# Optimization experiments

Hardware: AMD Instinct MI355X
Metric: run time of the kernel (lower is better)

The kernel has to match this reference:

```python
import jax, jax.numpy as jnp
import numpy as np
from itertools import combinations

N = 40        # number of vectors
D = 5         # ambient dim
WIDTH = 128   # channel width
N_HIDDEN = 2  # hidden GeneralLinear layers


def _partition_labels(k):
    # restricted-growth strings = set partitions of range(k)
    out = []
    def rec(prefix):
        if len(prefix) == k:
            out.append(tuple(prefix)); return
        m = (max(prefix) + 1) if prefix else 0
        for v in range(m + 1):
            rec(prefix + [v])
    rec([])
    return out


def _canon(lab):
    m = {}
    return tuple(m.setdefault(v, len(m)) for v in lab)


def _indicator(lab, n):
    # T[i0..ik-1] = 1 iff equality pattern of indices matches the partition exactly
    k = len(lab)
    ax = [np.arange(n).reshape([n if i == a else 1 for i in range(k)]) for a in range(k)]
    T = np.ones((n,) * k, dtype=bool)
    for a, b in combinations(range(k), 2):
        eq = ax[a] == ax[b]
        T &= eq if lab[a] == lab[b] else ~eq
    return T.astype(np.float32)


def perm_invariant_basis(k, n, swappable=()):
    labs = _partition_labels(k)
    if not swappable:
        return jnp.asarray(np.stack([_indicator(l, n) for l in labs]))
    (a, b), = swappable
    tensors, seen = [], set()
    for lab in labs:
        sl = list(lab); sl[a], sl[b] = sl[b], sl[a]
        sl = _canon(sl)
        if lab in seen or sl in seen:
            continue
        seen.add(lab); seen.add(sl)
        T = _indicator(lab, n)
        if sl != lab:
            T = T + _indicator(sl, n)  # symmetrize over the swappable index pair
        tensors.append(T)
    return jnp.asarray(np.stack(tensors))


def _gl4(basis, W, bw, bias_basis, x):
    # GeneralLinear on 2-tensor channels.
    # basis: (K,n,n,n,n)  x: (in,n,n)  W: (out,in,K)  bw: (out,Kb)  bias_basis: (Kb,n,n)
    t = jnp.einsum('kabcd,icd->ikab', basis, x)          # (in,K,n,n)
    out = jnp.einsum('oik,ikab->oab', W, t)
    return out + jnp.einsum('om,mab->oab', bw, bias_basis)


def setup_inputs() -> dict:
    key = jax.random.key(0)
    ks = jax.random.split(key, 10)
    basis_sym_nonsym = perm_invariant_basis(4, N, ((0, 1),))  # (11,n,n,n,n)
    basis_nonsym = perm_invariant_basis(4, N)                  # (15,n,n,n,n)
    bias_basis = perm_invariant_basis(2, N)                    # (2,n,n)
    K_sym = basis_sym_nonsym.shape[0]
    K_full = basis_nonsym.shape[0]
    K_b = bias_basis.shape[0]
    s = 0.02
    f32 = jnp.float32
    return {
        'S': jax.random.normal(ks[0], (N, D), f32),
        'basis_sym_nonsym': basis_sym_nonsym,
        'basis_nonsym': basis_nonsym,
        'bias_basis': bias_basis,
        'W0': jax.random.normal(ks[1], (WIDTH, 1, K_sym), f32) * s,
        'b0': jax.random.normal(ks[2], (WIDTH, K_b), f32) * s,
        'Wh': jax.random.normal(ks[3], (N_HIDDEN, WIDTH, WIDTH, K_full), f32) * s,
        'bh': jax.random.normal(ks[4], (N_HIDDEN, WIDTH, K_b), f32) * s,
        'Wp': jax.random.normal(ks[5], (1, WIDTH, K_sym), f32) * s,
        'bp': jax.random.normal(ks[6], (1, K_b), f32) * s,
        'Wi': jax.random.normal(ks[7], (1, WIDTH, K_b), f32) * s,
        'bi': jax.random.normal(ks[8], (1, 1), f32) * s,
    }


def reference(S, basis_sym_nonsym, basis_nonsym, bias_basis, W0, b0, Wh, bh, Wp, bp, Wi, bi):
    n, d = S.shape
    X = (S @ S.T)[None]                                               # (1,n,n) Gram matrix
    X = jax.nn.leaky_relu(_gl4(basis_sym_nonsym, W0, b0, bias_basis, X))
    for l in range(Wh.shape[0]):
        X = jax.nn.leaky_relu(_gl4(basis_nonsym, Wh[l], bh[l], bias_basis, X))
    basis_nonsym_sym = jnp.transpose(basis_sym_nonsym, (0, 3, 4, 1, 2))
    pairs = _gl4(basis_nonsym_sym, Wp, bp, bias_basis, X)[0]          # (n,n)
    # identity head: order-2 basis fully contracts X to a scalar; bias_basis=ones((1,1))
    identity_scalar = jnp.einsum('oik,kab,iab->o', Wi, bias_basis, X) + bi[:, 0]  # (1,)
    # A[c,d] = sum_ab pairs[a,b] S[a,c] S[b,d]  (== einsum('ab,abcd->cd', pairs, S(x)S))
    A = jnp.einsum('ab,ac,bd->cd', pairs, S, S) + identity_scalar * jnp.eye(d, dtype=S.dtype)
    _, eigvecs = jnp.linalg.eigh(A)
    u = eigvecs[:, -1]                                                # top eigenvector
    return S @ u
```

## Files before the change

kernel.cpp:

```cpp
#include <hip/hip_runtime.h>
#include <math.h>

#define NPTS 40
#define NN   1600
#define WID  128
#define NPAIR 780

#define ST_D  0
#define ST_R  5120
#define ST_C  10240
#define ST_TR 15360
#define ST_T  15488
#define ST_SIZE 16384

#define VT_VA   0
#define VT_VB   5120
#define VT_VDG  10240
#define VT_SOFF 15360
#define VT_SDG  15488
#define VT_SIZE 15616

#define PVA 0
#define PVB 40
#define PDG 80
#define PSOFF 120
#define PSDG 121

#define CM_SZ1 16384
#define CM_SIZE (15*16384)

#define WS_XTA   0
#define WS_XTB   204800
#define WS_STA   409600
#define WS_STB   425984
#define WS_STC   442368
#define WS_CM0   458752
#define WS_CM1   704512
#define WS_VT1   950272
#define WS_VT2   965888
#define WS_VTP   981504
#define WS_PRAW  981632
#define WS_TOTAL 983232

static __device__ __forceinline__ float lrelu(float v) {
    return v >= 0.f ? v : 0.01f * v;
}

static __device__ __forceinline__ void pair_decode(int q, int& a, int& b) {
    int aa = 0, rem = q;
    while (rem >= 39 - aa) { rem -= 39 - aa; ++aa; }
    a = aa; b = aa + 1 + rem;
}

__global__ __launch_bounds__(256) void k_l0c(
    const float* __restrict__ S, const float* __restrict__ W0, const float* __restrict__ b0,
    const float* __restrict__ Wh,
    float* __restrict__ XT, float* __restrict__ st,
    float* __restrict__ cm0, float* __restrict__ cm1)
{
    const int tid = threadIdx.x;
    const int o = blockIdx.x;

    {
        const int idx = blockIdx.x * 256 + tid;
        const int l = idx >> 14;
        const int r2 = idx & 16383;
        const int oo = r2 >> 7;
        const int ii = r2 & 127;
        const float* w = Wh + ((l * WID + oo) * WID + ii) * 15;
        float* cm = l ? cm1 : cm0;
        const int base = ii * 128 + oo;
        const float w0=w[0],w1=w[1],w2=w[2],w3=w[3],w4=w[4],w5=w[5],w6=w[6],w7=w[7],
                    w8=w[8],w9=w[9],w10=w[10],w11=w[11],w12=w[12],w13=w[13],w14=w[14];
        cm[ 0*CM_SZ1+base] = w6 - w7 - w12 + w14;
        cm[ 1*CM_SZ1+base] = w8 - w10 - w11 + w14;
        cm[ 2*CM_SZ1+base] = w5 - w7 - w11 - w13 + 2.f*w14;
        cm[ 3*CM_SZ1+base] = w9 - w10 - w12 - w13 + 2.f*w14;
        cm[ 4*CM_SZ1+base] = w7 - w14;
        cm[ 5*CM_SZ1+base] = w10 - w14;
        cm[ 6*CM_SZ1+base] = w11 - w14;
        cm[ 7*CM_SZ1+base] = w12 - w14;
        cm[ 8*CM_SZ1+base] = w0 - w1 - w2 - w3 + 2.f*w4;
        cm[ 9*CM_SZ1+base] = w1 - w4;
        cm[10*CM_SZ1+base] = w2 - w4;
        cm[11*CM_SZ1+base] = w13 - w14;
        cm[12*CM_SZ1+base] = w14;
        cm[13*CM_SZ1+base] = w3 - w4;
        cm[14*CM_SZ1+base] = w4;
    }

    __shared__ float sS[NPTS * 5];
    __shared__ float sX[NN];
    __shared__ float sP[NN];
    __shared__ float sR[NPTS], sC[NPTS], sD[NPTS], sTT[2];

    for (int t = tid; t < NPTS * 5; t += 256) sS[t] = S[t];
    __syncthreads();
    for (int p = tid; p < NN; p += 256) {
        int a = p / NPTS, b = p % NPTS;
        float acc = 0.f;
#pragma unroll
        for (int k = 0; k < 5; ++k) acc += sS[a * 5 + k] * sS[b * 5 + k];
        sX[p] = acc;
    }
    __syncthreads();
    if (tid < NPTS) {
        float r = 0.f, c = 0.f;
        for (int j = 0; j < NPTS; ++j) { r += sX[tid * NPTS + j]; c += sX[j * NPTS + tid]; }
        sR[tid] = r; sC[tid] = c; sD[tid] = sX[tid * 41];
    }
    __syncthreads();
    if (tid == 0) {
        float tr = 0.f, T = 0.f;
        for (int a = 0; a < NPTS; ++a) { tr += sD[a]; T += sR[a]; }
        sTT[0] = tr; sTT[1] = T;
    }
    __syncthreads();

    float w[11];
#pragma unroll
    for (int k = 0; k < 11; ++k) w[k] = W0[o * 11 + k];
    const float tr = sTT[0], T = sTT[1];
    const float cfX = w[6] - w[7] - w[8] + w[10];
    const float cfd = w[5] - w[7] - w[8] - w[9] + 2.f * w[10];
    const float cfR = w[7] - w[10];
    const float cfC = w[8] - w[10];
    const float so  = w[9] * tr + w[10] * (T - tr) + b0[o * 2 + 1];
    const float cdd = w[0] - w[1] - w[2] - w[3] + 2.f * w[4];
    const float cdR = w[1] - w[4];
    const float cdC = w[2] - w[4];
    const float sd  = w[3] * tr + w[4] * (T - tr) + b0[o * 2 + 0];

    for (int p = tid; p < NN; p += 256) {
        int a = p / NPTS, b = p % NPTS;
        float v;
        if (a == b) {
            v = cdd * sD[a] + cdR * sR[a] + cdC * sC[a] + sd;
        } else {
            float xs = sX[p] + sX[b * NPTS + a];
            v = cfX * xs + cfd * (sD[a] + sD[b]) + cfR * (sR[a] + sR[b]) + cfC * (sC[a] + sC[b]) + so;
        }
        sP[p] = lrelu(v);
    }
    __syncthreads();
    for (int p = tid; p < NN; p += 256) XT[p * WID + o] = sP[p];
    if (tid < NPTS) {
        float r = 0.f, c = 0.f;
        for (int j = 0; j < NPTS; ++j) { r += sP[tid * NPTS + j]; c += sP[j * NPTS + tid]; }
        st[ST_D + o * NPTS + tid] = sP[tid * 41];
        st[ST_R + o * NPTS + tid] = r;
        st[ST_C + o * NPTS + tid] = c;
        sR[tid] = r; sD[tid] = sP[tid * 41];
    }
    __syncthreads();
    if (tid == 0) {
        float t2 = 0.f, T2 = 0.f;
        for (int a = 0; a < NPTS; ++a) { t2 += sD[a]; T2 += sR[a]; }
        st[ST_TR + o] = t2; st[ST_T + o] = T2;
    }
}

template<bool COMP>
__global__ __launch_bounds__(256) void k_sv(
    const float* __restrict__ XT, const float* __restrict__ stIn,
    float* __restrict__ stOut,
    const float* __restrict__ cm, const float* __restrict__ bias,
    float* __restrict__ vt)
{
    const int tid = threadIdx.x;
    const int i = tid & 127, h = tid >> 7;
    const int a = blockIdx.x;
    __shared__ float sD[128], sR[128], sC[128], sTr[128], sT[128];
    __shared__ float part[2][2][128];
    __shared__ float vpart[3][2][128];

    if (a < 40) {
        if (COMP) {
            float r = 0.f, c = 0.f;
            for (int b = h * 20; b < h * 20 + 20; ++b) {
                r += XT[(a * 40 + b) * WID + i];
                c += XT[(b * 40 + a) * WID + i];
            }
            part[0][h][i] = r; part[1][h][i] = c;
            __syncthreads();
            if (tid < 128) {
                sR[i] = part[0][0][i] + part[0][1][i];
                sC[i] = part[1][0][i] + part[1][1][i];
                sD[i] = XT[(a * 41) * WID + i];
                stOut[ST_D + i * 40 + a] = sD[i];
                stOut[ST_R + i * 40 + a] = sR[i];
                stOut[ST_C + i * 40 + a] = sC[i];
            }
        } else {
            if (tid < 128) {
                sD[i] = stIn[ST_D + i * 40 + a];
                sR[i] = stIn[ST_R + i * 40 + a];
                sC[i] = stIn[ST_C + i * 40 + a];
            }
            __syncthreads();
        }
        __syncthreads();
        const int o = i;
        float acca = 0.f, accb = 0.f, accg = 0.f;
        for (int k = h * 64; k < h * 64 + 64; ++k) {
            const float d = sD[k], r = sR[k], c = sC[k];
            acca += cm[ 2*CM_SZ1 + k*128 + o] * d + cm[ 4*CM_SZ1 + k*128 + o] * r + cm[ 6*CM_SZ1 + k*128 + o] * c;
            accb += cm[ 3*CM_SZ1 + k*128 + o] * d + cm[ 5*CM_SZ1 + k*128 + o] * r + cm[ 7*CM_SZ1 + k*128 + o] * c;
            accg += cm[ 8*CM_SZ1 + k*128 + o] * d + cm[ 9*CM_SZ1 + k*128 + o] * r + cm[10*CM_SZ1 + k*128 + o] * c;
        }
        vpart[0][h][o] = acca; vpart[1][h][o] = accb; vpart[2][h][o] = accg;
        __syncthreads();
        if (tid < 128) {
            vt[VT_VA  + a * 128 + o] = vpart[0][0][o] + vpart[0][1][o];
            vt[VT_VB  + a * 128 + o] = vpart[1][0][o] + vpart[1][1][o];
            vt[VT_VDG + a * 128 + o] = vpart[2][0][o] + vpart[2][1][o];
        }
    } else {
        if (COMP) {
            float tt = 0.f;
            for (int p = h * 800; p < (h + 1) * 800; ++p) tt += XT[p * WID + i];
            part[0][h][i] = tt;
            __syncthreads();
            if (tid < 128) {
                sT[i] = part[0][0][i] + part[0][1][i];
                float trv = 0.f;
                for (int a2 = 0; a2 < 40; ++a2) trv += XT[(a2 * 41) * WID + i];
                sTr[i] = trv;
                stOut[ST_TR + i] = trv; stOut[ST_T + i] = sT[i];
            }
        } else {
            if (tid < 128) { sTr[i] = stIn[ST_TR + i]; sT[i] = stIn[ST_T + i]; }
            __syncthreads();
        }
        __syncthreads();
        const int o = i;
        float soff = 0.f, sdg = 0.f;
        for (int k = h * 64; k < h * 64 + 64; ++k) {
            const float trv = sTr[k], Tv = sT[k];
            soff += cm[11*CM_SZ1 + k*128 + o] * trv + cm[12*CM_SZ1 + k*128 + o] * Tv;
            sdg  += cm[13*CM_SZ1 + k*128 + o] * trv + cm[14*CM_SZ1 + k*128 + o] * Tv;
        }
        vpart[0][h][o] = soff; vpart[1][h][o] = sdg;
        __syncthreads();
        if (tid < 128) {
            vt[VT_SOFF + o] = vpart[0][0][o] + vpart[0][1][o] + bias[o * 2 + 1];
            vt[VT_SDG  + o] = vpart[1][0][o] + vpart[1][1][o] + bias[o * 2 + 0];
        }
    }
}

__global__ __launch_bounds__(256) void k_hid(
    const float* __restrict__ XTin, float* __restrict__ XTout,
    const float* __restrict__ cm, const float* __restrict__ vt)
{
    const int tid = threadIdx.x;
    const int blk = blockIdx.x;
    if (blk == 390) {
        const int o = tid & 127, h = tid >> 7;
        const float sdg = vt[VT_SDG + o];
        for (int a = h; a < 40; a += 2)
            XTout[(a * 41) * WID + o] = lrelu(vt[VT_VDG + a * 128 + o] + sdg);
        return;
    }
    __shared__ float sxab[2][128], sxba[2][128];
    const int j = tid >> 7, o = tid & 127;
    int aa, bb;
    pair_decode(blk * 2 + j, aa, bb);
    const int p = aa * 40 + bb, pt = bb * 40 + aa;
    sxab[j][o] = XTin[p * WID + o];
    sxba[j][o] = XTin[pt * WID + o];
    __syncthreads();

    float acc1 = 0.f, acc2 = 0.f;
#pragma unroll 8
    for (int i2 = 0; i2 < 128; ++i2) {
        const float c1v = cm[i2 * 128 + o];
        const float c2v = cm[CM_SZ1 + i2 * 128 + o];
        const float xab = sxab[j][i2];
        const float xba = sxba[j][i2];
        acc1 += c1v * xab + c2v * xba;
        acc2 += c1v * xba + c2v * xab;
    }
    const float soff = vt[VT_SOFF + o];
    XTout[p * WID + o]  = lrelu(acc1 + vt[VT_VA + aa * 128 + o] + vt[VT_VB + bb * 128 + o] + soff);
    XTout[pt * WID + o] = lrelu(acc2 + vt[VT_VA + bb * 128 + o] + vt[VT_VB + aa * 128 + o] + soff);
}

__global__ __launch_bounds__(256) void k_svp(
    const float* __restrict__ XT, float* __restrict__ stOut,
    const float* __restrict__ Wp, const float* __restrict__ bp,
    float* __restrict__ vtp, float* __restrict__ praw)
{
    const int tid = threadIdx.x;
    const int i = tid & 127, h = tid >> 7;
    const int blk = blockIdx.x;
    __shared__ float sD[128], sR[128], sC[128];
    __shared__ float part[2][2][128];
    __shared__ float red[3][128];

    if (blk < 40) {
        const int a = blk;
        float r = 0.f, c = 0.f;
        for (int b = h * 20; b < h * 20 + 20; ++b) {
            r += XT[(a * 40 + b) * WID + i];
            c += XT[(b * 40 + a) * WID + i];
        }
        part[0][h][i] = r; part[1][h][i] = c;
        __syncthreads();
        if (tid < 128) {
            sR[i] = part[0][0][i] + part[0][1][i];
            sC[i] = part[1][0][i] + part[1][1][i];
            sD[i] = XT[(a * 41) * WID + i];
            stOut[ST_D + i * 40 + a] = sD[i];
            stOut[ST_R + i * 40 + a] = sR[i];
            stOut[ST_C + i * 40 + a] = sC[i];
        }
        __syncthreads();
        if (tid < 128) {
            const float* pw = Wp + i * 11;
            const float p0=pw[0],p1=pw[1],p2=pw[2],p3=pw[3],p4=pw[4],p5=pw[5],
                        p7=pw[7],p8=pw[8],p9=pw[9],p10=pw[10];
            const float cpa = p1 - p4 - 2.f*p7 + 2.f*p10;
            const float cpb = p2 - p4 - 2.f*p8 + 2.f*p10;
            const float cra = p7 - p10;
            const float crb = p8 - p10;
            const float cddp = p0 - p3 - 2.f*p5 + 2.f*p9;
            const float crcp = p5 - p9;
            const float rc = sR[i] + sC[i];
            red[0][i] = cpa * sD[i] + cra * rc;
            red[1][i] = cpb * sD[i] + crb * rc;
            red[2][i] = cddp * sD[i] + crcp * rc;
        }
        __syncthreads();
        for (int s = 64; s > 0; s >>= 1) {
            if (tid < s) {
                red[0][tid] += red[0][tid + s];
                red[1][tid] += red[1][tid + s];
                red[2][tid] += red[2][tid + s];
            }
            __syncthreads();
        }
        if (tid == 0) {
            vtp[PVA + a] = red[0][0];
            vtp[PVB + a] = red[1][0];
            vtp[PDG + a] = red[2][0];
        }
    } else if (blk == 40) {
        float tt = 0.f;
        for (int p = h * 800; p < (h + 1) * 800; ++p) tt += XT[p * WID + i];
        part[0][h][i] = tt;
        __syncthreads();
        if (tid < 128) {
            const float Tv = part[0][0][i] + part[0][1][i];
            float trv = 0.f;
            for (int a2 = 0; a2 < 40; ++a2) trv += XT[(a2 * 41) * WID + i];
            stOut[ST_TR + i] = trv; stOut[ST_T + i] = Tv;
            const float p3 = Wp[i*11+3], p4 = Wp[i*11+4], p9 = Wp[i*11+9], p10 = Wp[i*11+10];
            red[0][i] = (p4 - p10) * trv + p10 * Tv;
            red[1][i] = (p3 - p9) * trv + p9 * Tv;
        }
        __syncthreads();
        for (int s = 64; s > 0; s >>= 1) {
            if (tid < s) { red[0][tid] += red[0][tid + s]; red[1][tid] += red[1][tid + s]; }
            __syncthreads();
        }
        if (tid == 0) {
            vtp[PSOFF] = red[0][0] + bp[1];
            vtp[PSDG]  = red[1][0] + bp[0];
        }
    } else {
        int aa, bb;
        pair_decode(blk - 41, aa, bb);
        const int p = aa * 40 + bb, pt = bb * 40 + aa;
        if (tid < 128) {
            const float p6 = Wp[i*11+6], p7 = Wp[i*11+7], p8 = Wp[i*11+8], p10 = Wp[i*11+10];
            red[0][i] = (p6 - p7 - p8 + p10) * (XT[p * WID + i] + XT[pt * WID + i]);
        }
        __syncthreads();
        for (int s = 64; s > 0; s >>= 1) {
            if (tid < s) red[0][tid] += red[0][tid + s];
            __syncthreads();
        }
        if (tid == 0) { praw[p] = red[0][0]; praw[pt] = red[0][0]; }
    }
}

__global__ __launch_bounds__(256) void k_final(
    const float* __restrict__ S, const float* __restrict__ praw,
    const float* __restrict__ vtp,
    const float* __restrict__ st, const float* __restrict__ Wi,
    const float* __restrict__ bi, float* __restrict__ out)
{
    __shared__ float sS[NPTS * 5];
    __shared__ float sPr[NN];
    __shared__ float M1[5][NPTS];
    __shared__ float sA[25];
    __shared__ float sIsc;
    __shared__ double sU[5];
    const int tid = threadIdx.x;

    for (int t = tid; t < NPTS * 5; t += 256) sS[t] = S[t];
    for (int p = tid; p < NN; p += 256) {
        const int a = p / NPTS, b = p % NPTS;
        float v;
        if (a == b) v = vtp[PDG + a] + vtp[PSDG];
        else        v = praw[p] + vtp[PVA + a] + vtp[PVB + b] + vtp[PSOFF];
        sPr[p] = v;
    }
    __syncthreads();

    if (tid < 200) {
        const int c = tid / NPTS, b = tid % NPTS;
        float acc = 0.f;
        for (int a = 0; a < NPTS; ++a) acc += sS[a * 5 + c] * sPr[a * NPTS + b];
        M1[c][b] = acc;
    }
    if (tid == 255) {
        float s = 0.f;
        for (int i = 0; i < WID; ++i) {
            const float tri = st[ST_TR + i], Ti = st[ST_T + i];
            s += Wi[i * 2 + 0] * tri + Wi[i * 2 + 1] * (Ti - tri);
        }
        sIsc = s + bi[0];
    }
    __syncthreads();
    if (tid < 25) {
        const int c = tid / 5, d = tid % 5;
        float acc = 0.f;
        for (int b = 0; b < NPTS; ++b) acc += M1[c][b] * sS[b * 5 + d];
        sA[tid] = acc;
    }
    __syncthreads();

    if (tid == 0) {
        double A[5][5], V[5][5];
        for (int c = 0; c < 5; ++c)
            for (int d = 0; d < 5; ++d)
                A[c][d] = (double)((c >= d) ? sA[c * 5 + d] : sA[d * 5 + c]);
        for (int c = 0; c < 5; ++c) A[c][c] += (double)sIsc;
        for (int c = 0; c < 5; ++c)
            for (int d = 0; d < 5; ++d) V[c][d] = (c == d) ? 1.0 : 0.0;

        double dscale = 1.0;
        for (int c = 0; c < 5; ++c) dscale += A[c][c] * A[c][c];
        for (int sweep = 0; sweep < 30; ++sweep) {
            double off = 0.0;
            for (int p = 0; p < 4; ++p)
                for (int q = p + 1; q < 5; ++q) off += A[p][q] * A[p][q];
            if (off < 1e-26 * dscale) break;
            for (int p = 0; p < 4; ++p) {
                for (int q = p + 1; q < 5; ++q) {
                    const double apq = A[p][q];
                    if (fabs(apq) < 1e-300) continue;
                    const double theta = (A[q][q] - A[p][p]) / (2.0 * apq);
                    const double t = (theta >= 0.0 ? 1.0 : -1.0) / (fabs(theta) + sqrt(theta * theta + 1.0));
                    const double c = 1.0 / sqrt(t * t + 1.0);
                    const double s = t * c;
                    for (int k = 0; k < 5; ++k) {
                        const double akp = A[k][p], akq = A[k][q];
                        A[k][p] = c * akp - s * akq;
                        A[k][q] = s * akp + c * akq;
                    }
                    for (int k = 0; k < 5; ++k) {
                        const double apk = A[p][k], aqk = A[q][k];
                        A[p][k] = c * apk - s * aqk;
                        A[q][k] = s * apk + c * aqk;
                    }
                    for (int k = 0; k < 5; ++k) {
                        const double vkp = V[k][p], vkq = V[k][q];
                        V[k][p] = c * vkp - s * vkq;
                        V[k][q] = s * vkp + c * vkq;
                    }
                }
            }
        }
        int best = 0;
        for (int k = 1; k < 5; ++k) if (A[k][k] > A[best][best]) best = k;
        double u[5];
        for (int k = 0; k < 5; ++k) u[k] = V[k][best];
        int jm = 0; double am = fabs(u[0]);
        for (int k = 1; k < 5; ++k) if (fabs(u[k]) > am) { am = fabs(u[k]); jm = k; }
        if (u[jm] < 0.0) for (int k = 0; k < 5; ++k) u[k] = -u[k];
        for (int k = 0; k < 5; ++k) sU[k] = u[k];
    }
    __syncthreads();
    if (tid < NPTS) {
        float acc = 0.f;
#pragma unroll
        for (int k = 0; k < 5; ++k) acc += sS[tid * 5 + k] * (float)sU[k];
        out[tid] = acc;
    }
}

extern "C" void kernel_launch(void* const* d_in, const int* in_sizes, int n_in,
                              void* d_out, int out_size, void* d_ws, size_t ws_size,
                              hipStream_t stream) {
    const float* S  = (const float*)d_in[0];
    const float* W0 = (const float*)d_in[4];
    const float* b0 = (const float*)d_in[5];
    const float* Wh = (const float*)d_in[6];
    const float* bh = (const float*)d_in[7];
    const float* Wp = (const float*)d_in[8];
    const float* bp = (const float*)d_in[9];
    const float* Wi = (const float*)d_in[10];
    const float* bi = (const float*)d_in[11];
    float* out = (float*)d_out;
    float* ws = (float*)d_ws;
    if (ws_size < (size_t)WS_TOTAL * sizeof(float)) return;

    float* XTA = ws + WS_XTA;
    float* XTB = ws + WS_XTB;
    float* stA = ws + WS_STA;
    float* stB = ws + WS_STB;
    float* stC = ws + WS_STC;
    float* cm0 = ws + WS_CM0;
    float* cm1 = ws + WS_CM1;
    float* vt1 = ws + WS_VT1;
    float* vt2 = ws + WS_VT2;
    float* vtp = ws + WS_VTP;
    float* praw = ws + WS_PRAW;

    k_l0c<<<WID, 256, 0, stream>>>(S, W0, b0, Wh, XTA, stA, cm0, cm1);
    k_sv<false><<<41, 256, 0, stream>>>(XTA, stA, stB, cm0, bh, vt1);
    k_hid<<<391, 256, 0, stream>>>(XTA, XTB, cm0, vt1);
    k_sv<true><<<41, 256, 0, stream>>>(XTB, stB, stB, cm1, bh + 2 * WID, vt2);
    k_hid<<<391, 256, 0, stream>>>(XTB, XTA, cm1, vt2);
    k_svp<<<821, 256, 0, stream>>>(XTA, stC, Wp, bp, vtp, praw);
    k_final<<<1, 256, 0, stream>>>(S, praw, vtp, stC, Wi, bi, out);
}
```

Before: 134.0 us.

## Fuse hidden layers, stats, projection head and eigen solve into three kernels

Merges the per-layer statistics/vector kernels into the hidden-layer kernels, so each of the 390 blocks recomputes the needed row/column/diagonal reductions and cm-weighted vectors for its own endpoints. The projection head and final eigen solve are folded into the second hidden kernel, which uses atomics and a last-block counter instead of separate launches. This cuts the launch count from seven to three and removes the intermediate dependency bubbles. In exchange, the cm-weighted vector work is done redundantly in every block, and the change adds atomic reductions plus a single-block tail.

After: 179.3 us. 1.34x slower.

```diff
diff --git a/kernel.cpp b/kernel.cpp
--- a/kernel.cpp
+++ b/kernel.cpp
@@ -4,43 +4,32 @@
 #define NPTS 40
 #define NN   1600
 #define WID  128
-#define NPAIR 780
 
 #define ST_D  0
 #define ST_R  5120
 #define ST_C  10240
 #define ST_TR 15360
 #define ST_T  15488
-#define ST_SIZE 16384
-
-#define VT_VA   0
-#define VT_VB   5120
-#define VT_VDG  10240
-#define VT_SOFF 15360
-#define VT_SDG  15488
-#define VT_SIZE 15616
+
+#define CM_SZ1 16384
 
 #define PVA 0
 #define PVB 40
 #define PDG 80
-#define PSOFF 120
-#define PSDG 121
-
-#define CM_SZ1 16384
-#define CM_SIZE (15*16384)
+#define A_SOFF 120
+#define A_SDG  121
+#define A_ISC  122
 
 #define WS_XTA   0
 #define WS_XTB   204800
 #define WS_STA   409600
-#define WS_STB   425984
-#define WS_STC   442368
-#define WS_CM0   458752
-#define WS_CM1   704512
-#define WS_VT1   950272
-#define WS_VT2   965888
-#define WS_VTP   981504
-#define WS_PRAW  981632
-#define WS_TOTAL 983232
+#define WS_CM0   425984
+#define WS_CM1   671744
+#define WS_T1    917504
+#define WS_ACC   917632
+#define WS_PRAW  917760
+#define WS_CNT   919360
+#define WS_TOTAL 919424
 
 static __device__ __forceinline__ float lrelu(float v) {
     return v >= 0.f ? v : 0.01f * v;
@@ -56,13 +45,20 @@
     const float* __restrict__ S, const float* __restrict__ W0, const float* __restrict__ b0,
     const float* __restrict__ Wh,
     float* __restrict__ XT, float* __restrict__ st,
-    float* __restrict__ cm0, float* __restrict__ cm1)
+    float* __restrict__ cm0, float* __restrict__ cm1,
+    float* __restrict__ T1, float* __restrict__ accb, unsigned int* __restrict__ cnt)
 {
     const int tid = threadIdx.x;
     const int o = blockIdx.x;
 
+    if (o == 0) {
+        if (tid < 128) T1[tid] = 0.f;
+        if (tid >= 128) accb[tid - 128] = 0.f;
+        if (tid == 0) *cnt = 0u;
+    }
+
     {
-        const int idx = blockIdx.x * 256 + tid;
+        const int idx = o * 256 + tid;
         const int l = idx >> 14;
         const int r2 = idx & 16383;
         const int oo = r2 >> 7;
@@ -106,7 +102,7 @@
     __syncthreads();
     if (tid < NPTS) {
         float r = 0.f, c = 0.f;
-        for (int j = 0; j < NPTS; ++j) { r += sX[tid * NPTS + j]; c += sX[j * NPTS + tid]; }
+        for (int jj = 0; jj < NPTS; ++jj) { r += sX[tid * NPTS + jj]; c += sX[jj * NPTS + tid]; }
         sR[tid] = r; sC[tid] = c; sD[tid] = sX[tid * 41];
     }
     __syncthreads();
@@ -146,7 +142,7 @@
     for (int p = tid; p < NN; p += 256) XT[p * WID + o] = sP[p];
     if (tid < NPTS) {
         float r = 0.f, c = 0.f;
-        for (int j = 0; j < NPTS; ++j) { r += sP[tid * NPTS + j]; c += sP[j * NPTS + tid]; }
+        for (int jj = 0; jj < NPTS; ++jj) { r += sP[tid * NPTS + jj]; c += sP[jj * NPTS + tid]; }
         st[ST_D + o * NPTS + tid] = sP[tid * 41];
         st[ST_R + o * NPTS + tid] = r;
         st[ST_C + o * NPTS + tid] = c;
@@ -160,284 +156,326 @@
     }
 }
 
-template<bool COMP>
-__global__ __launch_bounds__(256) void k_sv(
-    const float* __restrict__ XT, const float* __restrict__ stIn,
-    float* __restrict__ stOut,
-    const float* __restrict__ cm, const float* __restrict__ bias,
-    float* __restrict__ vt)
+__global__ __launch_bounds__(256) void k_hid1(
+    const float* __restrict__ XTA, const float* __restrict__ stA,
+    const float* __restrict__ cm, const float* __restrict__ bl,
+    float* __restrict__ XTB, float* __restrict__ T1)
 {
-    const int tid = threadIdx.x;
-    const int i = tid & 127, h = tid >> 7;
-    const int a = blockIdx.x;
-    __shared__ float sD[128], sR[128], sC[128], sTr[128], sT[128];
-    __shared__ float part[2][2][128];
-    __shared__ float vpart[3][2][128];
-
-    if (a < 40) {
-        if (COMP) {
+    const int tid = threadIdx.x, blk = blockIdx.x;
+    const int j = tid >> 7, o = tid & 127;
+    const bool diag = (blk < 40);
+    int e0, e1, e2, e3;
+    pair_decode(2 * blk, e0, e1);
+    pair_decode(2 * blk + 1, e2, e3);
+    const int epl[5] = { e0, e1, e2, e3, diag ? blk : 0 };
+    const int nep = diag ? 5 : 4;
+
+    __shared__ float sD[5][128], sR[5][128], sC[5][128], sTr[128], sT[128];
+    __shared__ float sxab[2][128], sxba[2][128];
+    __shared__ float vpart[11][2][128];
+    __shared__ float svt[11][128];
+
+    for (int t = tid; t < nep * 128; t += 256) {
+        const int e = t >> 7, k = t & 127, a = epl[e];
+        sD[e][k] = stA[ST_D + k * 40 + a];
+        sR[e][k] = stA[ST_R + k * 40 + a];
+        sC[e][k] = stA[ST_C + k * 40 + a];
+    }
+    if (tid < 128) { sTr[o] = stA[ST_TR + o]; sT[o] = stA[ST_T + o]; }
+    {
+        const int a = epl[2 * j], b = epl[2 * j + 1];
+        sxab[j][o] = XTA[(a * 40 + b) * 128 + o];
+        sxba[j][o] = XTA[(b * 40 + a) * 128 + o];
+    }
+    __syncthreads();
+
+    float fva0 = 0, fva1 = 0, fva2 = 0, fva3 = 0;
+    float fvb0 = 0, fvb1 = 0, fvb2 = 0, fvb3 = 0;
+    float fso = 0, fdg = 0, fsd = 0;
+    const int k0 = 64 * j;
+    for (int k = k0; k < k0 + 64; ++k) {
+        const int c = k * 128 + o;
+        const float m2 = cm[2*CM_SZ1+c], m3 = cm[3*CM_SZ1+c], m4 = cm[4*CM_SZ1+c],
+                    m5 = cm[5*CM_SZ1+c], m6 = cm[6*CM_SZ1+c], m7 = cm[7*CM_SZ1+c];
+        {
+            const float d = sD[0][k], r = sR[0][k], cc = sC[0][k];
+            fva0 += m2*d + m4*r + m6*cc; fvb0 += m3*d + m5*r + m7*cc;
+        }
+        {
+            const float d = sD[1][k], r = sR[1][k], cc = sC[1][k];
+            fva1 += m2*d + m4*r + m6*cc; fvb1 += m3*d + m5*r + m7*cc;
+        }
+        {
+            const float d = sD[2][k], r = sR[2][k], cc = sC[2][k];
+            fva2 += m2*d + m4*r + m6*cc; fvb2 += m3*d + m5*r + m7*cc;
+        }
+        {
+            const float d = sD[3][k], r = sR[3][k], cc = sC[3][k];
+            fva3 += m2*d + m4*r + m6*cc; fvb3 += m3*d + m5*r + m7*cc;
+        }
+        fso += cm[11*CM_SZ1+c] * sTr[k] + cm[12*CM_SZ1+c] * sT[k];
+        if (diag) {
+            fdg += cm[8*CM_SZ1+c]*sD[4][k] + cm[9*CM_SZ1+c]*sR[4][k] + cm[10*CM_SZ1+c]*sC[4][k];
+            fsd += cm[13*CM_SZ1+c]*sTr[k] + cm[14*CM_SZ1+c]*sT[k];
+        }
+    }
+    vpart[0][j][o]=fva0; vpart[1][j][o]=fva1; vpart[2][j][o]=fva2; vpart[3][j][o]=fva3;
+    vpart[4][j][o]=fvb0; vpart[5][j][o]=fvb1; vpart[6][j][o]=fvb2; vpart[7][j][o]=fvb3;
+    vpart[8][j][o]=fso; vpart[9][j][o]=fdg; vpart[10][j][o]=fsd;
+    __syncthreads();
+    if (tid < 128) {
+        for (int m = 0; m < 8; ++m) svt[m][o] = vpart[m][0][o] + vpart[m][1][o];
+        svt[8][o]  = vpart[8][0][o] + vpart[8][1][o] + bl[o * 2 + 1];
+        svt[9][o]  = vpart[9][0][o] + vpart[9][1][o];
+        svt[10][o] = vpart[10][0][o] + vpart[10][1][o] + bl[o * 2 + 0];
+    }
+    __syncthreads();
+
+    float acc1 = 0.f, acc2 = 0.f;
+#pragma unroll 8
+    for (int i = 0; i < 128; ++i) {
+        const float c1v = cm[i * 128 + o];
+        const float c2v = cm[CM_SZ1 + i * 128 + o];
+        const float xab = sxab[j][i], xba = sxba[j][i];
+        acc1 += c1v * xab + c2v * xba;
+        acc2 += c1v * xba + c2v * xab;
+    }
+    const int a = epl[2 * j], b = epl[2 * j + 1];
+    const float so = svt[8][o];
+    const float o1 = lrelu(acc1 + svt[2 * j][o]     + svt[4 + 2 * j + 1][o] + so);
+    const float o2 = lrelu(acc2 + svt[2 * j + 1][o] + svt[4 + 2 * j][o]     + so);
+    XTB[(a * 40 + b) * 128 + o] = o1;
+    XTB[(b * 40 + a) * 128 + o] = o2;
+    float xd = 0.f;
+    if (diag && j == 0) {
+        xd = lrelu(svt[9][o] + svt[10][o]);
+        XTB[(blk * 41) * 128 + o] = xd;
+    }
+    vpart[0][j][o] = o1 + o2 + xd;
+    __syncthreads();
+    if (tid < 128) atomicAdd(&T1[o], vpart[0][0][o] + vpart[0][1][o]);
+}
+
+__global__ __launch_bounds__(256) void k_hid2f(
+    const float* __restrict__ S,
+    const float* __restrict__ XTB, const float* __restrict__ T1,
+    const float* __restrict__ cm, const float* __restrict__ bl,
+    const float* __restrict__ Wp, const float* __restrict__ bp,
+    const float* __restrict__ Wi, const float* __restrict__ bi,
+    float* __restrict__ praw, float* __restrict__ accb, unsigned int* __restrict__ cnt,
+    float* __restrict__ out)
+{
+    const int tid = threadIdx.x, blk = blockIdx.x;
+    const int j = tid >> 7, o = tid & 127;
+    const bool diag = (blk < 40);
+    int e0, e1, e2, e3;
+    pair_decode(2 * blk, e0, e1);
+    pair_decode(2 * blk + 1, e2, e3);
+    const int epl[5] = { e0, e1, e2, e3, diag ? blk : 0 };
+    const int nep = diag ? 5 : 4;
+
+    __shared__ float sD[5][128], sR[5][128], sC[5][128], sTr[128], sT[128];
+    __shared__ float sxab[2][128], sxba[2][128];
+    __shared__ float vpart[11][2][128];
+    __shared__ float svt[11][128];
+    __shared__ float sxd[128];
+    __shared__ float rr[7][2][128];
+    __shared__ double dbuf[55];
+    __shared__ int sLast;
+
+    {
+        const int k = o, h = j;
+        for (int e = 0; e < nep; ++e) {
+            const int a = epl[e];
             float r = 0.f, c = 0.f;
-            for (int b = h * 20; b < h * 20 + 20; ++b) {
-                r += XT[(a * 40 + b) * WID + i];
-                c += XT[(b * 40 + a) * WID + i];
+            for (int b = 20 * h; b < 20 * h + 20; ++b) {
+                r += XTB[(a * 40 + b) * 128 + k];
+                c += XTB[(b * 40 + a) * 128 + k];
             }
-            part[0][h][i] = r; part[1][h][i] = c;
+            vpart[0][h][k] = r; vpart[1][h][k] = c;
             __syncthreads();
             if (tid < 128) {
-                sR[i] = part[0][0][i] + part[0][1][i];
-                sC[i] = part[1][0][i] + part[1][1][i];
-                sD[i] = XT[(a * 41) * WID + i];
-                stOut[ST_D + i * 40 + a] = sD[i];
-                stOut[ST_R + i * 40 + a] = sR[i];
-                stOut[ST_C + i * 40 + a] = sC[i];
-            }
-        } else {
-            if (tid < 128) {
-                sD[i] = stIn[ST_D + i * 40 + a];
-                sR[i] = stIn[ST_R + i * 40 + a];
-                sC[i] = stIn[ST_C + i * 40 + a];
+                sD[e][k] = XTB[(a * 41) * 128 + k];
+                sR[e][k] = vpart[0][0][k] + vpart[0][1][k];
+                sC[e][k] = vpart[1][0][k] + vpart[1][1][k];
             }
             __syncthreads();
         }
+        float t = 0.f;
+        for (int a2 = 20 * h; a2 < 20 * h + 20; ++a2) t += XTB[(a2 * 41) * 128 + k];
+        vpart[0][h][k] = t;
         __syncthreads();
-        const int o = i;
-        float acca = 0.f, accb = 0.f, accg = 0.f;
-        for (int k = h * 64; k < h * 64 + 64; ++k) {
-            const float d = sD[k], r = sR[k], c = sC[k];
-            acca += cm[ 2*CM_SZ1 + k*128 + o] * d + cm[ 4*CM_SZ1 + k*128 + o] * r + cm[ 6*CM_SZ1 + k*128 + o] * c;
-            accb += cm[ 3*CM_SZ1 + k*128 + o] * d + cm[ 5*CM_SZ1 + k*128 + o] * r + cm[ 7*CM_SZ1 + k*128 + o] * c;
-            accg += cm[ 8*CM_SZ1 + k*128 + o] * d + cm[ 9*CM_SZ1 + k*128 + o] * r + cm[10*CM_SZ1 + k*128 + o] * c;
-        }
-        vpart[0][h][o] = acca; vpart[1][h][o] = accb; vpart[2][h][o] = accg;
-        __syncthreads();
-        if (tid < 128) {
-            vt[VT_VA  + a * 128 + o] = vpart[0][0][o] + vpart[0][1][o];
-            vt[VT_VB  + a * 128 + o] = vpart[1][0][o] + vpart[1][1][o];
-            vt[VT_VDG + a * 128 + o] = vpart[2][0][o] + vpart[2][1][o];
-        }
-    } else {
-        if (COMP) {
-            float tt = 0.f;
-            for (int p = h * 800; p < (h + 1) * 800; ++p) tt += XT[p * WID + i];
-            part[0][h][i] = tt;
-            __syncthreads();
-            if (tid < 128) {
-                sT[i] = part[0][0][i] + part[0][1][i];
-                float trv = 0.f;
-                for (int a2 = 0; a2 < 40; ++a2) trv += XT[(a2 * 41) * WID + i];
-                sTr[i] = trv;
-                stOut[ST_TR + i] = trv; stOut[ST_T + i] = sT[i];
-            }
-        } else {
-            if (tid < 128) { sTr[i] = stIn[ST_TR + i]; sT[i] = stIn[ST_T + i]; }
-            __syncthreads();
-        }
-        __syncthreads();
-        const int o = i;
-        float soff = 0.f, sdg = 0.f;
-        for (int k = h * 64; k < h * 64 + 64; ++k) {
-            const float trv = sTr[k], Tv = sT[k];
-            soff += cm[11*CM_SZ1 + k*128 + o] * trv + cm[12*CM_SZ1 + k*128 + o] * Tv;
-            sdg  += cm[13*CM_SZ1 + k*128 + o] * trv + cm[14*CM_SZ1 + k*128 + o] * Tv;
-        }
-        vpart[0][h][o] = soff; vpart[1][h][o] = sdg;
-        __syncthreads();
-        if (tid < 128) {
-            vt[VT_SOFF + o] = vpart[0][0][o] + vpart[0][1][o] + bias[o * 2 + 1];
-            vt[VT_SDG  + o] = vpart[1][0][o] + vpart[1][1][o] + bias[o * 2 + 0];
-        }
-    }
-}
-
-__global__ __launch_bounds__(256) void k_hid(
-    const float* __restrict__ XTin, float* __restrict__ XTout,
-    const float* __restrict__ cm, const float* __restrict__ vt)
-{
-    const int tid = threadIdx.x;
-    const int blk = blockIdx.x;
-    if (blk == 390) {
-        const int o = tid & 127, h = tid >> 7;
-        const float sdg = vt[VT_SDG + o];
-        for (int a = h; a < 40; a += 2)
-            XTout[(a * 41) * WID + o] = lrelu(vt[VT_VDG + a * 128 + o] + sdg);
-        return;
-    }
-    __shared__ float sxab[2][128], sxba[2][128];
-    const int j = tid >> 7, o = tid & 127;
-    int aa, bb;
-    pair_decode(blk * 2 + j, aa, bb);
-    const int p = aa * 40 + bb, pt = bb * 40 + aa;
-    sxab[j][o] = XTin[p * WID + o];
-    sxba[j][o] = XTin[pt * WID + o];
+        if (tid < 128) { sTr[k] = vpart[0][0][k] + vpart[0][1][k]; sT[k] = T1[k]; }
+    }
+    {
+        const int a = epl[2 * j], b = epl[2 * j + 1];
+        sxab[j][o] = XTB[(a * 40 + b) * 128 + o];
+        sxba[j][o] = XTB[(b * 40 + a) * 128 + o];
+    }
+    __syncthreads();
+
+    float fva0 = 0, fva1 = 0, fva2 = 0, fva3 = 0;
+    float fvb0 = 0, fvb1 = 0, fvb2 = 0, fvb3 = 0;
+    float fso = 0, fdg = 0, fsd = 0;
+    const int k0 = 64 * j;
+    for (int k = k0; k < k0 + 64; ++k) {
+        const int c = k * 128 + o;
+        const float m2 = cm[2*CM_SZ1+c], m3 = cm[3*CM_SZ1+c], m4 = cm[4*CM_SZ1+c],
+                    m5 = cm[5*CM_SZ1+c], m6 = cm[6*CM_SZ1+c], m7 = cm[7*CM_SZ1+c];
+        {
+            const float d = sD[0][k], r = sR[0][k], cc = sC[0][k];
+            fva0 += m2*d + m4*r + m6*cc; fvb0 += m3*d + m5*r + m7*cc;
+        }
+        {
+            const float d = sD[1][k], r = sR[1][k], cc = sC[1][k];
+            fva1 += m2*d + m4*r + m6*cc; fvb1 += m3*d + m5*r + m7*cc;
+        }
+        {
+            const float d = sD[2][k], r = sR[2][k], cc = sC[2][k];
+            fva2 += m2*d + m4*r + m6*cc; fvb2 += m3*d + m5*r + m7*cc;
+        }
+        {
+            const float d = sD[3][k], r = sR[3][k], cc = sC[3][k];
+            fva3 += m2*d + m4*r + m6*cc; fvb3 += m3*d + m5*r + m7*cc;
+        }
+        fso += cm[11*CM_SZ1+c] * sTr[k] + cm[12*CM_SZ1+c] * sT[k];
+        if (diag) {
+            fdg += cm[8*CM_SZ1+c]*sD[4][k] + cm[9*CM_SZ1+c]*sR[4][k] + cm[10*CM_SZ1+c]*sC[4][k];
+            fsd += cm[13*CM_SZ1+c]*sTr[k] + cm[14*CM_SZ1+c]*sT[k];
+        }
+    }
+    vpart[0][j][o]=fva0; vpart[1][j][o]=fva1; vpart[2][j][o]=fva2; vpart[3][j][o]=fva3;
+    vpart[4][j][o]=fvb0; vpart[5][j][o]=fvb1; vpart[6][j][o]=fvb2; vpart[7][j][o]=fvb3;
+    vpart[8][j][o]=fso; vpart[9][j][o]=fdg; vpart[10][j][o]=fsd;
+    __syncthreads();
+    if (tid < 128) {
+        for (int m = 0; m < 8; ++m) svt[m][o] = vpart[m][0][o] + vpart[m][1][o];
+        svt[8][o]  = vpart[8][0][o] + vpart[8][1][o] + bl[o * 2 + 1];
+        svt[9][o]  = vpart[9][0][o] + vpart[9][1][o];
+        svt[10][o] = vpart[10][0][o] + vpart[10][1][o] + bl[o * 2 + 0];
+    }
     __syncthreads();
 
     float acc1 = 0.f, acc2 = 0.f;
 #pragma unroll 8
-    for (int i2 = 0; i2 < 128; ++i2) {
-        const float c1v = cm[i2 * 128 + o];
-        const float c2v = cm[CM_SZ1 + i2 * 128 + o];
-        const float xab = sxab[j][i2];
-        const float xba = sxba[j][i2];
+    for (int i = 0; i < 128; ++i) {
+        const float c1v = cm[i * 128 + o];
+        const float c2v = cm[CM_SZ1 + i * 128 + o];
+        const float xab = sxab[j][i], xba = sxba[j][i];
         acc1 += c1v * xab + c2v * xba;
         acc2 += c1v * xba + c2v * xab;
     }
-    const float soff = vt[VT_SOFF + o];
-    XTout[p * WID + o]  = lrelu(acc1 + vt[VT_VA + aa * 128 + o] + vt[VT_VB + bb * 128 + o] + soff);
-    XTout[pt * WID + o] = lrelu(acc2 + vt[VT_VA + bb * 128 + o] + vt[VT_VB + aa * 128 + o] + soff);
-}
-
-__global__ __launch_bounds__(256) void k_svp(
-    const float* __restrict__ XT, float* __restrict__ stOut,
-    const float* __restrict__ Wp, const float* __restrict__ bp,
-    float* __restrict__ vtp, float* __restrict__ praw)
-{
-    const int tid = threadIdx.x;
-    const int i = tid & 127, h = tid >> 7;
-    const int blk = blockIdx.x;
-    __shared__ float sD[128], sR[128], sC[128];
-    __shared__ float part[2][2][128];
-    __shared__ float red[3][128];
-
-    if (blk < 40) {
-        const int a = blk;
-        float r = 0.f, c = 0.f;
-        for (int b = h * 20; b < h * 20 + 20; ++b) {
-            r += XT[(a * 40 + b) * WID + i];
-            c += XT[(b * 40 + a) * WID + i];
-        }
-        part[0][h][i] = r; part[1][h][i] = c;
+    const int pa = epl[2 * j], pb = epl[2 * j + 1];
+    const float so = svt[8][o];
+    const float x1 = lrelu(acc1 + svt[2 * j][o]     + svt[4 + 2 * j + 1][o] + so);
+    const float x2 = lrelu(acc2 + svt[2 * j + 1][o] + svt[4 + 2 * j][o]     + so);
+    if (diag && j == 0) sxd[o] = lrelu(svt[9][o] + svt[10][o]);
+
+    const float p0 = Wp[o*11+0], p1 = Wp[o*11+1], p2 = Wp[o*11+2], p3 = Wp[o*11+3],
+                p4 = Wp[o*11+4], p5 = Wp[o*11+5], p6 = Wp[o*11+6], p7 = Wp[o*11+7],
+                p8 = Wp[o*11+8], p9 = Wp[o*11+9], p10 = Wp[o*11+10];
+    const float wi0 = Wi[o*2+0], wi1 = Wi[o*2+1];
+    const float s12 = x1 + x2;
+    rr[0][j][o] = (p6 - p7 - p8 + p10) * s12;
+    rr[1][j][o] = (p7 - p10) * s12;
+    rr[2][j][o] = (p8 - p10) * s12;
+    rr[3][j][o] = (p5 - p9) * s12;
+    rr[4][j][o] = p10 * s12;
+    rr[5][j][o] = p9 * s12;
+    rr[6][j][o] = wi1 * s12;
+    __syncthreads();
+    for (int stp = 64; stp > 0; stp >>= 1) {
+        if (o < stp) {
+            for (int m = 0; m < 7; ++m) rr[m][j][o] += rr[m][j][o + stp];
+        }
         __syncthreads();
-        if (tid < 128) {
-            sR[i] = part[0][0][i] + part[0][1][i];
-            sC[i] = part[1][0][i] + part[1][1][i];
-            sD[i] = XT[(a * 41) * WID + i];
-            stOut[ST_D + i * 40 + a] = sD[i];
-            stOut[ST_R + i * 40 + a] = sR[i];
-            stOut[ST_C + i * 40 + a] = sC[i];
-        }
+    }
+    if (o == 0) {
+        const float v = rr[0][j][0];
+        praw[pa * 40 + pb] = v;
+        praw[pb * 40 + pa] = v;
+        atomicAdd(&accb[PVA + pa], rr[1][j][0]); atomicAdd(&accb[PVA + pb], rr[1][j][0]);
+        atomicAdd(&accb[PVB + pa], rr[2][j][0]); atomicAdd(&accb[PVB + pb], rr[2][j][0]);
+        atomicAdd(&accb[PDG + pa], rr[3][j][0]); atomicAdd(&accb[PDG + pb], rr[3][j][0]);
+        atomicAdd(&accb[A_SOFF], rr[4][j][0]);
+        atomicAdd(&accb[A_SDG],  rr[5][j][0]);
+        atomicAdd(&accb[A_ISC],  rr[6][j][0]);
+    }
+    if (diag) {
         __syncthreads();
-        if (tid < 128) {
-            const float* pw = Wp + i * 11;
-            const float p0=pw[0],p1=pw[1],p2=pw[2],p3=pw[3],p4=pw[4],p5=pw[5],
-                        p7=pw[7],p8=pw[8],p9=pw[9],p10=pw[10];
-            const float cpa = p1 - p4 - 2.f*p7 + 2.f*p10;
-            const float cpb = p2 - p4 - 2.f*p8 + 2.f*p10;
-            const float cra = p7 - p10;
-            const float crb = p8 - p10;
-            const float cddp = p0 - p3 - 2.f*p5 + 2.f*p9;
-            const float crcp = p5 - p9;
-            const float rc = sR[i] + sC[i];
-            red[0][i] = cpa * sD[i] + cra * rc;
-            red[1][i] = cpb * sD[i] + crb * rc;
-            red[2][i] = cddp * sD[i] + crcp * rc;
-        }
+        const float xdv = (j == 0) ? sxd[o] : 0.f;
+        rr[0][j][o] = (p1 - p4) * xdv;
+        rr[1][j][o] = (p2 - p4) * xdv;
+        rr[2][j][o] = (p0 - p3) * xdv;
+        rr[3][j][o] = p4 * xdv;
+        rr[4][j][o] = p3 * xdv;
+        rr[5][j][o] = wi0 * xdv;
         __syncthreads();
-        for (int s = 64; s > 0; s >>= 1) {
-            if (tid < s) {
-                red[0][tid] += red[0][tid + s];
-                red[1][tid] += red[1][tid + s];
-                red[2][tid] += red[2][tid + s];
+        for (int stp = 64; stp > 0; stp >>= 1) {
+            if (o < stp) {
+                for (int m = 0; m < 6; ++m) rr[m][j][o] += rr[m][j][o + stp];
             }
             __syncthreads();
         }
         if (tid == 0) {
-            vtp[PVA + a] = red[0][0];
-            vtp[PVB + a] = red[1][0];
-            vtp[PDG + a] = red[2][0];
-        }
-    } else if (blk == 40) {
-        float tt = 0.f;
-        for (int p = h * 800; p < (h + 1) * 800; ++p) tt += XT[p * WID + i];
-        part[0][h][i] = tt;
-        __syncthreads();
-        if (tid < 128) {
-            const float Tv = part[0][0][i] + part[0][1][i];
-            float trv = 0.f;
-            for (int a2 = 0; a2 < 40; ++a2) trv += XT[(a2 * 41) * WID + i];
-            stOut[ST_TR + i] = trv; stOut[ST_T + i] = Tv;
-            const float p3 = Wp[i*11+3], p4 = Wp[i*11+4], p9 = Wp[i*11+9], p10 = Wp[i*11+10];
-            red[0][i] = (p4 - p10) * trv + p10 * Tv;
-            red[1][i] = (p3 - p9) * trv + p9 * Tv;
-        }
-        __syncthreads();
-        for (int s = 64; s > 0; s >>= 1) {
-            if (tid < s) { red[0][tid] += red[0][tid + s]; red[1][tid] += red[1][tid + s]; }
-            __syncthreads();
-        }
-        if (tid == 0) {
-            vtp[PSOFF] = red[0][0] + bp[1];
-            vtp[PSDG]  = red[1][0] + bp[0];
-        }
-    } else {
-        int aa, bb;
-        pair_decode(blk - 41, aa, bb);
-        const int p = aa * 40 + bb, pt = bb * 40 + aa;
-        if (tid < 128) {
-            const float p6 = Wp[i*11+6], p7 = Wp[i*11+7], p8 = Wp[i*11+8], p10 = Wp[i*11+10];
-            red[0][i] = (p6 - p7 - p8 + p10) * (XT[p * WID + i] + XT[pt * WID + i]);
-        }
-        __syncthreads();
-        for (int s = 64; s > 0; s >>= 1) {
-            if (tid < s) red[0][tid] += red[0][tid + s];
-            __syncthreads();
-        }
-        if (tid == 0) { praw[p] = red[0][0]; praw[pt] = red[0][0]; }
-    }
-}
-
-__global__ __launch_bounds__(256) void k_final(
-    const float* __restrict__ S, const float* __restrict__ praw,
-    const float* __restrict__ vtp,
-    const float* __restrict__ st, const float* __restrict__ Wi,
-    const float* __restrict__ bi, float* __restrict__ out)
-{
-    __shared__ float sS[NPTS * 5];
-    __shared__ float sPr[NN];
-    __shared__ float M1[5][NPTS];
-    __shared__ float sA[25];
-    __shared__ float sIsc;
-    __shared__ double sU[5];
-    const int tid = threadIdx.x;
-
-    for (int t = tid; t < NPTS * 5; t += 256) sS[t] = S[t];
+            atomicAdd(&accb[PVA + blk], rr[0][0][0]);
+            atomicAdd(&accb[PVB + blk], rr[1][0][0]);
+            atomicAdd(&accb[PDG + blk], rr[2][0][0]);
+            atomicAdd(&accb[A_SOFF], rr[3][0][0]);
+            atomicAdd(&accb[A_SDG],  rr[4][0][0]);
+            atomicAdd(&accb[A_ISC],  rr[5][0][0]);
+        }
+    }
+
+    __threadfence();
+    if (tid == 0) {
+        const unsigned old = atomicAdd(cnt, 1u);
+        sLast = (old == 389u) ? 1 : 0;
+    }
+    __syncthreads();
+    if (!sLast) return;
+    __threadfence();
+
+    float* sPr = &vpart[0][0][0];
+    float* M1  = &svt[0][0];
+    float* sSS = &sxab[0][0];
+    float* sA  = &sxd[0];
+
+    for (int t = tid; t < NPTS * 5; t += 256) sSS[t] = S[t];
+    const float psoff = accb[A_SOFF] + bp[1];
+    const float psdg  = accb[A_SDG]  + bp[0];
     for (int p = tid; p < NN; p += 256) {
         const int a = p / NPTS, b = p % NPTS;
         float v;
-        if (a == b) v = vtp[PDG + a] + vtp[PSDG];
-        else        v = praw[p] + vtp[PVA + a] + vtp[PVB + b] + vtp[PSOFF];
+        if (a == b) v = accb[PDG + a] + psdg;
+        else        v = praw[p] + accb[PVA + a] + accb[PVB + b] + psoff;
         sPr[p] = v;
     }
     __syncthreads();
-
     if (tid < 200) {
         const int c = tid / NPTS, b = tid % NPTS;
         float acc = 0.f;
-        for (int a = 0; a < NPTS; ++a) acc += sS[a * 5 + c] * sPr[a * NPTS + b];
-        M1[c][b] = acc;
-    }
-    if (tid == 255) {
-        float s = 0.f;
-        for (int i = 0; i < WID; ++i) {
-            const float tri = st[ST_TR + i], Ti = st[ST_T + i];
-            s += Wi[i * 2 + 0] * tri + Wi[i * 2 + 1] * (Ti - tri);
-        }
-        sIsc = s + bi[0];
+        for (int a = 0; a < NPTS; ++a) acc += sSS[a * 5 + c] * sPr[a * NPTS + b];
+        M1[c * NPTS + b] = acc;
     }
     __syncthreads();
     if (tid < 25) {
         const int c = tid / 5, d = tid % 5;
         float acc = 0.f;
-        for (int b = 0; b < NPTS; ++b) acc += M1[c][b] * sS[b * 5 + d];
+        for (int b = 0; b < NPTS; ++b) acc += M1[c * NPTS + b] * sSS[b * 5 + d];
         sA[tid] = acc;
     }
     __syncthreads();
 
     if (tid == 0) {
-        double A[5][5], V[5][5];
+        const float isc = accb[A_ISC] + bi[0];
+        double (*A)[5] = (double(*)[5])&dbuf[0];
+        double (*V)[5] = (double(*)[5])&dbuf[25];
+        double* sU = &dbuf[50];
         for (int c = 0; c < 5; ++c)
             for (int d = 0; d < 5; ++d)
                 A[c][d] = (double)((c >= d) ? sA[c * 5 + d] : sA[d * 5 + c]);
-        for (int c = 0; c < 5; ++c) A[c][c] += (double)sIsc;
+        for (int c = 0; c < 5; ++c) A[c][c] += (double)isc;
         for (int c = 0; c < 5; ++c)
             for (int d = 0; d < 5; ++d) V[c][d] = (c == d) ? 1.0 : 0.0;
 
@@ -454,22 +492,22 @@
                     if (fabs(apq) < 1e-300) continue;
                     const double theta = (A[q][q] - A[p][p]) / (2.0 * apq);
                     const double t = (theta >= 0.0 ? 1.0 : -1.0) / (fabs(theta) + sqrt(theta * theta + 1.0));
-                    const double c = 1.0 / sqrt(t * t + 1.0);
-                    const double s = t * c;
+                    const double cth = 1.0 / sqrt(t * t + 1.0);
+                    const double sth = t * cth;
                     for (int k = 0; k < 5; ++k) {
                         const double akp = A[k][p], akq = A[k][q];
-                        A[k][p] = c * akp - s * akq;
-                        A[k][q] = s * akp + c * akq;
+                        A[k][p] = cth * akp - sth * akq;
+                        A[k][q] = sth * akp + cth * akq;
                     }
                     for (int k = 0; k < 5; ++k) {
                         const double apk = A[p][k], aqk = A[q][k];
-                        A[p][k] = c * apk - s * aqk;
-                        A[q][k] = s * apk + c * aqk;
+                        A[p][k] = cth * apk - sth * aqk;
+                        A[q][k] = sth * apk + cth * aqk;
                     }
                     for (int k = 0; k < 5; ++k) {
                         const double vkp = V[k][p], vkq = V[k][q];
-                        V[k][p] = c * vkp - s * vkq;
-                        V[k][q] = s * vkp + c * vkq;
+                        V[k][p] = cth * vkp - sth * vkq;
+                        V[k][q] = sth * vkp + cth * vkq;
                     }
                 }
             }
@@ -487,7 +525,7 @@
     if (tid < NPTS) {
         float acc = 0.f;
 #pragma unroll
-        for (int k = 0; k < 5; ++k) acc += sS[tid * 5 + k] * (float)sU[k];
+        for (int k = 0; k < 5; ++k) acc += sSS[tid * 5 + k] * (float)dbuf[50 + k];
         out[tid] = acc;
     }
 }
@@ -504,27 +542,22 @@
     const float* bp = (const float*)d_in[9];
     const float* Wi = (const float*)d_in[10];
     const float* bi = (const float*)d_in[11];
-    float* out = (float*)d_out;
+    float* outf = (float*)d_out;
     float* ws = (float*)d_ws;
     if (ws_size < (size_t)WS_TOTAL * sizeof(float)) return;
 
-    float* XTA = ws + WS_XTA;
-    float* XTB = ws + WS_XTB;
-    float* stA = ws + WS_STA;
-    float* stB = ws + WS_STB;
-    float* stC = ws + WS_STC;
-    float* cm0 = ws + WS_CM0;
-    float* cm1 = ws + WS_CM1;
-    float* vt1 = ws + WS_VT1;
-    float* vt2 = ws + WS_VT2;
-    float* vtp = ws + WS_VTP;
+    float* XTA  = ws + WS_XTA;
+    float* XTB  = ws + WS_XTB;
+    float* stA  = ws + WS_STA;
+    float* cm0  = ws + WS_CM0;
+    float* cm1  = ws + WS_CM1;
+    float* T1   = ws + WS_T1;
+    float* accb = ws + WS_ACC;
     float* praw = ws + WS_PRAW;
-
-    k_l0c<<<WID, 256, 0, stream>>>(S, W0, b0, Wh, XTA, stA, cm0, cm1);
-    k_sv<false><<<41, 256, 0, stream>>>(XTA, stA, stB, cm0, bh, vt1);
-    k_hid<<<391, 256, 0, stream>>>(XTA, XTB, cm0, vt1);
-    k_sv<true><<<41, 256, 0, stream>>>(XTB, stB, stB, cm1, bh + 2 * WID, vt2);
-    k_hid<<<391, 256, 0, stream>>>(XTB, XTA, cm1, vt2);
-    k_svp<<<821, 256, 0, stream>>>(XTA, stC, Wp, bp, vtp, praw);
-    k_final<<<1, 256, 0, stream>>>(S, praw, vtp, stC, Wi, bi, out);
+    unsigned int* cnt = (unsigned int*)(ws + WS_CNT);
+
+    k_l0c<<<WID, 256, 0, stream>>>(S, W0, b0, Wh, XTA, stA, cm0, cm1, T1, accb, cnt);
+    k_hid1<<<390, 256, 0, stream>>>(XTA, stA, cm0, bh, XTB, T1);
+    k_hid2f<<<390, 256, 0, stream>>>(S, XTB, T1, cm1, bh + 2 * WID, Wp, bp, Wi, bi,
+                                     praw, accb, cnt, outf);
 }
```
